# Optimization experiments

Measured on AMD Instinct MI355X. Metric: run time of the kernel, lower is better.

The kernel has to match this reference:

```python
import jax, jax.numpy as jnp
import numpy as np

N_USER = 100000
N_ITEM = 50000
N = N_USER + N_ITEM
D = 64
E = 2400000
LAYERS = 3
B = 4096


def setup_inputs() -> dict:
    key = jax.random.key(0)
    ks = jax.random.split(key, 10)
    user_emb = jax.random.normal(ks[0], (N_USER, D), dtype=jnp.float32) * 0.1
    item_emb = jax.random.normal(ks[1], (N_ITEM, D), dtype=jnp.float32) * 0.1
    graph_src = jax.random.randint(ks[2], (E,), 0, N, dtype=jnp.int32)
    graph_dst = jax.random.randint(ks[3], (E,), 0, N, dtype=jnp.int32)
    # normalized adjacency values ~ 1/deg
    graph_val = jax.random.uniform(ks[4], (E,), dtype=jnp.float32) / 16.0
    sim_src = jax.random.randint(ks[5], (E,), 0, N, dtype=jnp.int32)
    sim_dst = jax.random.randint(ks[6], (E,), 0, N, dtype=jnp.int32)
    sim_val = jax.random.uniform(ks[7], (E,), dtype=jnp.float32) / 16.0
    users = jax.random.randint(ks[8], (B,), 0, N_USER, dtype=jnp.int32)
    items = jax.random.randint(ks[9], (B,), 0, N_ITEM, dtype=jnp.int32)
    return {"user_emb": user_emb, "item_emb": item_emb,
            "graph_src": graph_src, "graph_dst": graph_dst, "graph_val": graph_val,
            "sim_src": sim_src, "sim_dst": sim_dst, "sim_val": sim_val,
            "users": users, "items": items}


def _spmm(src, dst, val, emb):
    # out[dst] += val * emb[src]  -> sparse (N,N) @ (N,D)
    return jax.ops.segment_sum(val[:, None] * emb[src], dst, num_segments=N)


def _computer(user_emb, item_emb, graph_src, graph_dst, graph_val,
              sim_src, sim_dst, sim_val):
    all_emb = jnp.concatenate([user_emb, item_emb], axis=0)  # [N, D]
    embs = [all_emb]
    for _ in range(LAYERS):
        side_emb = _spmm(graph_src, graph_dst, graph_val, all_emb)  # residual=False
        similarity_emb = _spmm(sim_src, sim_dst, sim_val, all_emb)
        att_side = jnp.exp(jnp.mean(side_emb * all_emb + side_emb, axis=1))
        att_sim = jnp.exp(jnp.mean(similarity_emb * all_emb + similarity_emb, axis=1))
        denom = att_side + att_sim
        all_emb = (att_side / denom)[:, None] * side_emb + (att_sim / denom)[:, None] * similarity_emb
        embs.append(all_emb)
    light_out = jnp.mean(jnp.stack(embs, axis=1), axis=1)  # [N, D]
    return light_out[:N_USER], light_out[N_USER:]


def reference(user_emb, item_emb, graph_src, graph_dst, graph_val,
              sim_src, sim_dst, sim_val, users, items):
    all_users, all_items = _computer(user_emb, item_emb, graph_src, graph_dst,
                                     graph_val, sim_src, sim_dst, sim_val)
    users_emb = all_users[users]  # [B, D]
    items_emb = all_items[items]  # [B, D]
    return jnp.sum(users_emb * items_emb, axis=1)  # [B]
```

## Files before the change

kernel.cpp:

```cpp
#include <hip/hip_runtime.h>
#include <hip/hip_fp16.h>

#define N_USER 100000
#define N_ITEM 50000
#define NTOT   150000
#define D      64
#define NE     2400000
#define LAYERS 3
#define BB     4096

#define NBUCK  586
#define BCAP   6144
#define PART_EDGES 6912
#define PART_GRID  ((NE + PART_EDGES - 1) / PART_EDGES)

__device__ __forceinline__ float4 h4_to_f4(uint2 u) {
    __half2 h0 = *reinterpret_cast<__half2*>(&u.x);
    __half2 h1 = *reinterpret_cast<__half2*>(&u.y);
    float2 f0 = __half22float2(h0);
    float2 f1 = __half22float2(h1);
    return make_float4(f0.x, f0.y, f1.x, f1.y);
}
__device__ __forceinline__ uint2 f4_to_h4(float4 v) {
    __half2 h0 = __float22half2_rn(make_float2(v.x, v.y));
    __half2 h1 = __float22half2_rn(make_float2(v.z, v.w));
    uint2 u;
    u.x = *reinterpret_cast<unsigned*>(&h0);
    u.y = *reinterpret_cast<unsigned*>(&h1);
    return u;
}

__global__ __launch_bounds__(256) void init_emb(const float* __restrict__ ue,
                                                const float* __restrict__ ie,
                                                float4* __restrict__ cur0,
                                                uint2*  __restrict__ cur0h) {
    int i = blockIdx.x * blockDim.x + threadIdx.x;
    const int total = NTOT * 16;
    if (i >= total) return;
    const int userElems = N_USER * 16;
    float4 v = (i < userElems) ? ((const float4*)ue)[i]
                               : ((const float4*)ie)[i - userElems];
    cur0[i]  = v;
    cur0h[i] = f4_to_h4(v);
}

__global__ __launch_bounds__(256) void partition_edges(const int*   __restrict__ gsrc,
                                                       const int*   __restrict__ gdst,
                                                       const float* __restrict__ gval,
                                                       const int*   __restrict__ ssrc,
                                                       const int*   __restrict__ sdst,
                                                       const float* __restrict__ sval,
                                                       int*  __restrict__ bucketCount,
                                                       int2* __restrict__ bucketBuf) {
    __shared__ int2 stage[PART_EDGES];
    __shared__ unsigned short bucketOf[PART_EDGES];
    __shared__ int hist[NBUCK];
    __shared__ int localBase[NBUCK];
    __shared__ int gbase[NBUCK];
    __shared__ int tsum[256];

    const int setS = (blockIdx.x >= PART_GRID) ? 1 : 0;
    const int* __restrict__ src = setS ? ssrc : gsrc;
    const int* __restrict__ dst = setS ? sdst : gdst;
    const float* __restrict__ val = setS ? sval : gval;
    const int co = setS * NBUCK;
    int bb = blockIdx.x - setS * PART_GRID;
    int lo = bb * PART_EDGES;
    int hi = min(NE, lo + PART_EDGES);
    int cnt = hi - lo;
    int tid = threadIdx.x;

    for (int i = tid; i < NBUCK; i += 256) hist[i] = 0;
    __syncthreads();
    for (int i = lo + tid; i < hi; i += 256)
        atomicAdd(&hist[dst[i] >> 8], 1);
    __syncthreads();

    int b0 = tid * 3;
    int c0 = (b0 + 0 < NBUCK) ? hist[b0 + 0] : 0;
    int c1 = (b0 + 1 < NBUCK) ? hist[b0 + 1] : 0;
    int c2 = (b0 + 2 < NBUCK) ? hist[b0 + 2] : 0;
    int mysum = c0 + c1 + c2;
    tsum[tid] = mysum;
    __syncthreads();
    #pragma unroll
    for (int off = 1; off < 256; off <<= 1) {
        int t = (tid >= off) ? tsum[tid - off] : 0;
        __syncthreads();
        tsum[tid] += t;
        __syncthreads();
    }
    int texcl = tsum[tid] - mysum;
    if (b0 + 0 < NBUCK) localBase[b0 + 0] = texcl;
    if (b0 + 1 < NBUCK) localBase[b0 + 1] = texcl + c0;
    if (b0 + 2 < NBUCK) localBase[b0 + 2] = texcl + c0 + c1;
    if (b0 + 0 < NBUCK) gbase[b0 + 0] = c0 ? atomicAdd(&bucketCount[co + b0 + 0], c0) : 0;
    if (b0 + 1 < NBUCK) gbase[b0 + 1] = c1 ? atomicAdd(&bucketCount[co + b0 + 1], c1) : 0;
    if (b0 + 2 < NBUCK) gbase[b0 + 2] = c2 ? atomicAdd(&bucketCount[co + b0 + 2], c2) : 0;
    __syncthreads();
    for (int i = tid; i < NBUCK; i += 256) hist[i] = localBase[i];
    __syncthreads();

    for (int i = lo + tid; i < hi; i += 256) {
        int d = dst[i];
        int b = d >> 8;
        int r = atomicAdd(&hist[b], 1);
        stage[r] = make_int2(src[i] | ((d & 255) << 18), __float_as_int(val[i]));
        bucketOf[r] = (unsigned short)b;
    }
    __syncthreads();

    for (int j = tid; j < cnt; j += 256) {
        int b = bucketOf[j];
        int slot = gbase[b] + (j - localBase[b]);
        if (slot < BCAP)
            bucketBuf[(size_t)(co + b) * BCAP + slot] = stage[j];
    }
}

__global__ __launch_bounds__(1024) void scan_all(const int* __restrict__ bucketCount,
                                                 int* __restrict__ bucketBase,
                                                 int* __restrict__ rpG,
                                                 int* __restrict__ rpS) {
    __shared__ int s[1024];
    int tid = threadIdx.x;
    int c = (tid < NBUCK) ? bucketCount[tid] : 0;
    s[tid] = c;
    __syncthreads();
    #pragma unroll
    for (int off = 1; off < 1024; off <<= 1) {
        int t = (tid >= off) ? s[tid - off] : 0;
        __syncthreads();
        s[tid] += t;
        __syncthreads();
    }
    if (tid < NBUCK) bucketBase[tid] = s[tid] - c;
    __syncthreads();
    int c2 = (tid < NBUCK) ? bucketCount[NBUCK + tid] : 0;
    s[tid] = c2;
    __syncthreads();
    #pragma unroll
    for (int off = 1; off < 1024; off <<= 1) {
        int t = (tid >= off) ? s[tid - off] : 0;
        __syncthreads();
        s[tid] += t;
        __syncthreads();
    }
    if (tid < NBUCK) bucketBase[NBUCK + tid] = NE + s[tid] - c2;
    if (tid == 0) { rpG[NTOT] = NE; rpS[NTOT] = 2 * NE; }
}

__global__ __launch_bounds__(256) void bucket_build(const int2* __restrict__ bucketBuf,
                                                    const int*  __restrict__ bucketCount,
                                                    const int*  __restrict__ bucketBase,
                                                    int*  __restrict__ rpG,
                                                    int*  __restrict__ rpS,
                                                    int2* __restrict__ sv) {
    __shared__ int2 e[BCAP];
    __shared__ int rhist[256];
    __shared__ int rscan[256];
    int b    = blockIdx.x;
    int setS = (b >= NBUCK) ? 1 : 0;
    int lb   = b - setS * NBUCK;
    int cnt  = min(bucketCount[b], BCAP);
    int obase = bucketBase[b];
    const int2* in = &bucketBuf[(size_t)b * BCAP];
    int tid = threadIdx.x;

    for (int i = tid; i < cnt; i += 256) e[i] = in[i];
    rhist[tid] = 0;
    __syncthreads();
    for (int i = tid; i < cnt; i += 256)
        atomicAdd(&rhist[(e[i].x >> 18) & 255], 1);
    __syncthreads();
    int myc = rhist[tid];
    rscan[tid] = myc;
    __syncthreads();
    #pragma unroll
    for (int off = 1; off < 256; off <<= 1) {
        int t = (tid >= off) ? rscan[tid - off] : 0;
        __syncthreads();
        rscan[tid] += t;
        __syncthreads();
    }
    int excl = rscan[tid] - myc;
    int grow = lb * 256 + tid;
    if (grow < NTOT) (setS ? rpS : rpG)[grow] = obase + excl;
    rhist[tid] = excl;
    __syncthreads();
    for (int i = tid; i < cnt; i += 256) {
        int row = (e[i].x >> 18) & 255;
        int pos = obase + atomicAdd(&rhist[row], 1);
        sv[pos] = make_int2(e[i].x & 0x3ffff, e[i].y);
    }
}

__global__ __launch_bounds__(256) void layer_fused(const int2* __restrict__ svG,
                                                   const int*  __restrict__ rpG,
                                                   const int2* __restrict__ svS,
                                                   const int*  __restrict__ rpS,
                                                   const float4* __restrict__ cur4,
                                                   const uint2*  __restrict__ curh,
                                                   float4* __restrict__ nxt4,
                                                   uint2*  __restrict__ nxth) {
    const int tid = threadIdx.x;
    const int lane16 = tid & 15;
    int row = blockIdx.x * 16 + (tid >> 4);
    if (row >= NTOT) return;
    size_t idx = (size_t)row * 16 + lane16;

    int pG = rpG[row], eG = rpG[row + 1];
    int pS = rpS[row], eS = rpS[row + 1];
    float4 c = cur4[idx];
    float4 aG = make_float4(0.f, 0.f, 0.f, 0.f);
    float4 aS = make_float4(0.f, 0.f, 0.f, 0.f);

    while (pG + 4 <= eG && pS + 4 <= eS) {
        int2 g0 = svG[pG + 0];
        int2 g1 = svG[pG + 1];
        int2 g2 = svG[pG + 2];
        int2 g3 = svG[pG + 3];
        int2 s0 = svS[pS + 0];
        int2 s1 = svS[pS + 1];
        int2 s2 = svS[pS + 2];
        int2 s3 = svS[pS + 3];
        uint2 ug0 = curh[(size_t)g0.x * 16 + lane16];
        uint2 ug1 = curh[(size_t)g1.x * 16 + lane16];
        uint2 ug2 = curh[(size_t)g2.x * 16 + lane16];
        uint2 ug3 = curh[(size_t)g3.x * 16 + lane16];
        uint2 us0 = curh[(size_t)s0.x * 16 + lane16];
        uint2 us1 = curh[(size_t)s1.x * 16 + lane16];
        uint2 us2 = curh[(size_t)s2.x * 16 + lane16];
        uint2 us3 = curh[(size_t)s3.x * 16 + lane16];
        float4 xg0 = h4_to_f4(ug0);
        float4 xg1 = h4_to_f4(ug1);
        float4 xg2 = h4_to_f4(ug2);
        float4 xg3 = h4_to_f4(ug3);
        float4 xs0 = h4_to_f4(us0);
        float4 xs1 = h4_to_f4(us1);
        float4 xs2 = h4_to_f4(us2);
        float4 xs3 = h4_to_f4(us3);
        float vg0 = __int_as_float(g0.y), vg1 = __int_as_float(g1.y);
        float vg2 = __int_as_float(g2.y), vg3 = __int_as_float(g3.y);
        float vs0 = __int_as_float(s0.y), vs1 = __int_as_float(s1.y);
        float vs2 = __int_as_float(s2.y), vs3 = __int_as_float(s3.y);
        aG.x = fmaf(vg0, xg0.x, aG.x); aG.y = fmaf(vg0, xg0.y, aG.y);
        aG.z = fmaf(vg0, xg0.z, aG.z); aG.w = fmaf(vg0, xg0.w, aG.w);
        aG.x = fmaf(vg1, xg1.x, aG.x); aG.y = fmaf(vg1, xg1.y, aG.y);
        aG.z = fmaf(vg1, xg1.z, aG.z); aG.w = fmaf(vg1, xg1.w, aG.w);
        aG.x = fmaf(vg2, xg2.x, aG.x); aG.y = fmaf(vg2, xg2.y, aG.y);
        aG.z = fmaf(vg2, xg2.z, aG.z); aG.w = fmaf(vg2, xg2.w, aG.w);
        aG.x = fmaf(vg3, xg3.x, aG.x); aG.y = fmaf(vg3, xg3.y, aG.y);
        aG.z = fmaf(vg3, xg3.z, aG.z); aG.w = fmaf(vg3, xg3.w, aG.w);
        aS.x = fmaf(vs0, xs0.x, aS.x); aS.y = fmaf(vs0, xs0.y, aS.y);
        aS.z = fmaf(vs0, xs0.z, aS.z); aS.w = fmaf(vs0, xs0.w, aS.w);
        aS.x = fmaf(vs1, xs1.x, aS.x); aS.y = fmaf(vs1, xs1.y, aS.y);
        aS.z = fmaf(vs1, xs1.z, aS.z); aS.w = fmaf(vs1, xs1.w, aS.w);
        aS.x = fmaf(vs2, xs2.x, aS.x); aS.y = fmaf(vs2, xs2.y, aS.y);
        aS.z = fmaf(vs2, xs2.z, aS.z); aS.w = fmaf(vs2, xs2.w, aS.w);
        aS.x = fmaf(vs3, xs3.x, aS.x); aS.y = fmaf(vs3, xs3.y, aS.y);
        aS.z = fmaf(vs3, xs3.z, aS.z); aS.w = fmaf(vs3, xs3.w, aS.w);
        pG += 4; pS += 4;
    }
    for (; pG < eG; ++pG) {
        int2 m = svG[pG];
        float4 x = h4_to_f4(curh[(size_t)m.x * 16 + lane16]);
        float v = __int_as_float(m.y);
        aG.x = fmaf(v, x.x, aG.x); aG.y = fmaf(v, x.y, aG.y);
        aG.z = fmaf(v, x.z, aG.z); aG.w = fmaf(v, x.w, aG.w);
    }
    for (; pS < eS; ++pS) {
        int2 m = svS[pS];
        float4 x = h4_to_f4(curh[(size_t)m.x * 16 + lane16]);
        float v = __int_as_float(m.y);
        aS.x = fmaf(v, x.x, aS.x); aS.y = fmaf(v, x.y, aS.y);
        aS.z = fmaf(v, x.z, aS.z); aS.w = fmaf(v, x.w, aS.w);
    }

    float4 c1 = make_float4(c.x + 1.f, c.y + 1.f, c.z + 1.f, c.w + 1.f);
    float t1 = aG.x * c1.x + aG.y * c1.y + aG.z * c1.z + aG.w * c1.w;
    float t2 = aS.x * c1.x + aS.y * c1.y + aS.z * c1.z + aS.w * c1.w;
    #pragma unroll
    for (int off = 8; off; off >>= 1) {
        t1 += __shfl_xor(t1, off, 64);
        t2 += __shfl_xor(t2, off, 64);
    }
    float a1 = expf(t1 * (1.0f / 64.0f));
    float a2 = expf(t2 * (1.0f / 64.0f));
    float den = a1 + a2;
    float w1 = a1 / den;
    float w2 = a2 / den;
    float4 nv = make_float4(w1 * aG.x + w2 * aS.x, w1 * aG.y + w2 * aS.y,
                            w1 * aG.z + w2 * aS.z, w1 * aG.w + w2 * aS.w);
    nxt4[idx] = nv;
    nxth[idx] = f4_to_h4(nv);
}

__global__ __launch_bounds__(256) void final_dot(const float* __restrict__ c0,
                                                 const float* __restrict__ c1,
                                                 const float* __restrict__ c2,
                                                 const float* __restrict__ c3,
                                                 const int* __restrict__ users,
                                                 const int* __restrict__ items,
                                                 float* __restrict__ out) {
    const int lane = threadIdx.x & 63;
    int b = blockIdx.x * (blockDim.x >> 6) + (threadIdx.x >> 6);
    if (b >= BB) return;
    size_t ub = (size_t)users[b] * D + lane;
    size_t vb = (size_t)(N_USER + items[b]) * D + lane;
    float x = (c0[ub] + c1[ub] + c2[ub] + c3[ub]) * 0.25f;
    float y = (c0[vb] + c1[vb] + c2[vb] + c3[vb]) * 0.25f;
    float p = x * y;
    #pragma unroll
    for (int off = 32; off; off >>= 1) p += __shfl_xor(p, off, 64);
    if (lane == 0) out[b] = p;
}

extern "C" void kernel_launch(void* const* d_in, const int* in_sizes, int n_in,
                              void* d_out, int out_size, void* d_ws, size_t ws_size,
                              hipStream_t stream) {
    const float* ue   = (const float*)d_in[0];
    const float* ie   = (const float*)d_in[1];
    const int*   gsrc = (const int*)d_in[2];
    const int*   gdst = (const int*)d_in[3];
    const float* gval = (const float*)d_in[4];
    const int*   ssrc = (const int*)d_in[5];
    const int*   sdst = (const int*)d_in[6];
    const float* sval = (const float*)d_in[7];
    const int*   users = (const int*)d_in[8];
    const int*   items = (const int*)d_in[9];
    float* out = (float*)d_out;

    char* p = (char*)d_ws;
    auto carve = [&](size_t bytes) { char* r = p; p += (bytes + 255) & ~(size_t)255; return r; };
    const size_t rowElems = (size_t)NTOT * D;
    float* cur[LAYERS + 1];
    for (int l = 0; l <= LAYERS; ++l) cur[l] = (float*)carve(rowElems * 4);
    uint2* curh[2];
    curh[0] = (uint2*)carve(rowElems * 2);
    curh[1] = (uint2*)carve(rowElems * 2);
    int2*  svAll = (int2*)carve((size_t)2 * NE * 8);
    int*   rpG   = (int*)carve((size_t)(NTOT + 1) * 4);
    int*   rpS   = (int*)carve((size_t)(NTOT + 1) * 4);
    int*   bucketCount = (int*)carve((size_t)2 * NBUCK * 4);
    int*   bucketBase  = (int*)carve((size_t)2 * NBUCK * 4);
    int2*  bucketBuf = (int2*)cur[2];
    (void)ws_size;

    init_emb<<<(NTOT * 16 + 255) / 256, 256, 0, stream>>>(ue, ie,
                                                          (float4*)cur[0], curh[0]);

    hipMemsetAsync(bucketCount, 0, (size_t)2 * NBUCK * 4, stream);
    partition_edges<<<2 * PART_GRID, 256, 0, stream>>>(gsrc, gdst, gval,
                                                       ssrc, sdst, sval,
                                                       bucketCount, bucketBuf);
    scan_all<<<1, 1024, 0, stream>>>(bucketCount, bucketBase, rpG, rpS);
    bucket_build<<<2 * NBUCK, 256, 0, stream>>>(bucketBuf, bucketCount, bucketBase,
                                                rpG, rpS, svAll);

    for (int l = 0; l < LAYERS; ++l) {
        layer_fused<<<(NTOT + 15) / 16, 256, 0, stream>>>(svAll, rpG, svAll, rpS,
                                                          (const float4*)cur[l],
                                                          curh[l & 1],
                                                          (float4*)cur[l + 1],
                                                          curh[(l + 1) & 1]);
    }

    final_dot<<<BB / 4, 256, 0, stream>>>(cur[0], cur[1], cur[2], cur[3],
                                          users, items, out);
}
```

Baseline: 535.0 us.

## Replace atomic bucket allocation with count/column-scan/scatter partition passes

Splits edge partitioning into a histogram pass, a per-bucket column scan over block counts, and a scatter pass that uses precomputed per-block offsets. This replaces global atomics on bucketCount with deterministic prefix offsets and drops the memset, and it unrolls the dst/src/val loads by four for more memory parallelism. The cost is two extra kernel launches, a second read of dst, and a strided column read of the block-count matrix.

New measurement: 462.7 us. 1.16x faster.

```diff
diff --git a/kernel.cpp b/kernel.cpp
--- a/kernel.cpp
+++ b/kernel.cpp
@@ -44,17 +44,109 @@
     cur0h[i] = f4_to_h4(v);
 }
 
-__global__ __launch_bounds__(256) void partition_edges(const int*   __restrict__ gsrc,
-                                                       const int*   __restrict__ gdst,
-                                                       const float* __restrict__ gval,
-                                                       const int*   __restrict__ ssrc,
-                                                       const int*   __restrict__ sdst,
-                                                       const float* __restrict__ sval,
-                                                       int*  __restrict__ bucketCount,
-                                                       int2* __restrict__ bucketBuf) {
+__global__ __launch_bounds__(256) void count_edges(const int* __restrict__ gdst,
+                                                   const int* __restrict__ sdst,
+                                                   int* __restrict__ blockCounts) {
+    __shared__ int hist[NBUCK];
+    const int setS = (blockIdx.x >= PART_GRID) ? 1 : 0;
+    const int* __restrict__ dst = setS ? sdst : gdst;
+    int bb = blockIdx.x - setS * PART_GRID;
+    int lo = bb * PART_EDGES;
+    int hi = min(NE, lo + PART_EDGES);
+    int tid = threadIdx.x;
+    for (int i = tid; i < NBUCK; i += 256) hist[i] = 0;
+    __syncthreads();
+    int i = lo + tid;
+    for (; i + 768 < hi; i += 1024) {
+        int d0 = dst[i];
+        int d1 = dst[i + 256];
+        int d2 = dst[i + 512];
+        int d3 = dst[i + 768];
+        atomicAdd(&hist[d0 >> 8], 1);
+        atomicAdd(&hist[d1 >> 8], 1);
+        atomicAdd(&hist[d2 >> 8], 1);
+        atomicAdd(&hist[d3 >> 8], 1);
+    }
+    for (; i < hi; i += 256) atomicAdd(&hist[dst[i] >> 8], 1);
+    __syncthreads();
+    int* row = &blockCounts[((size_t)blockIdx.x) * NBUCK];
+    for (int j = tid; j < NBUCK; j += 256) row[j] = hist[j];
+}
+
+__global__ __launch_bounds__(256) void colscan(const int* __restrict__ blockCounts,
+                                               int* __restrict__ blockPrefix,
+                                               int* __restrict__ bucketCount) {
+    __shared__ int s[256];
+    int tid = threadIdx.x;
+    int sb  = blockIdx.x;
+    int setS = (sb >= NBUCK) ? 1 : 0;
+    int bucket = sb - setS * NBUCK;
+    int base = 0;
+    for (int c0 = 0; c0 < PART_GRID; c0 += 256) {
+        int idx = c0 + tid;
+        size_t off = ((size_t)(setS * PART_GRID + idx)) * NBUCK + bucket;
+        int v = (idx < PART_GRID) ? blockCounts[off] : 0;
+        s[tid] = v;
+        __syncthreads();
+        #pragma unroll
+        for (int o = 1; o < 256; o <<= 1) {
+            int t = (tid >= o) ? s[tid - o] : 0;
+            __syncthreads();
+            s[tid] += t;
+            __syncthreads();
+        }
+        if (idx < PART_GRID) blockPrefix[off] = base + s[tid] - v;
+        int tot = s[255];
+        __syncthreads();
+        base += tot;
+    }
+    if (tid == 0) bucketCount[sb] = base;
+}
+
+__global__ __launch_bounds__(1024) void scan_all(const int* __restrict__ bucketCount,
+                                                 int* __restrict__ bucketBase,
+                                                 int* __restrict__ rpG,
+                                                 int* __restrict__ rpS) {
+    __shared__ int s[1024];
+    int tid = threadIdx.x;
+    int c = (tid < NBUCK) ? bucketCount[tid] : 0;
+    s[tid] = c;
+    __syncthreads();
+    #pragma unroll
+    for (int off = 1; off < 1024; off <<= 1) {
+        int t = (tid >= off) ? s[tid - off] : 0;
+        __syncthreads();
+        s[tid] += t;
+        __syncthreads();
+    }
+    if (tid < NBUCK) bucketBase[tid] = s[tid] - c;
+    __syncthreads();
+    int c2 = (tid < NBUCK) ? bucketCount[NBUCK + tid] : 0;
+    s[tid] = c2;
+    __syncthreads();
+    #pragma unroll
+    for (int off = 1; off < 1024; off <<= 1) {
+        int t = (tid >= off) ? s[tid - off] : 0;
+        __syncthreads();
+        s[tid] += t;
+        __syncthreads();
+    }
+    if (tid < NBUCK) bucketBase[NBUCK + tid] = NE + s[tid] - c2;
+    if (tid == 0) { rpG[NTOT] = NE; rpS[NTOT] = 2 * NE; }
+}
+
+__global__ __launch_bounds__(256) void partition_scatter(const int*   __restrict__ gsrc,
+                                                         const int*   __restrict__ gdst,
+                                                         const float* __restrict__ gval,
+                                                         const int*   __restrict__ ssrc,
+                                                         const int*   __restrict__ sdst,
+                                                         const float* __restrict__ sval,
+                                                         const int*   __restrict__ blockCounts,
+                                                         const int*   __restrict__ blockPrefix,
+                                                         int2* __restrict__ bucketBuf) {
     __shared__ int2 stage[PART_EDGES];
     __shared__ unsigned short bucketOf[PART_EDGES];
-    __shared__ int hist[NBUCK];
+    __shared__ int cursor[NBUCK];
     __shared__ int localBase[NBUCK];
     __shared__ int gbase[NBUCK];
     __shared__ int tsum[256];
@@ -69,17 +161,12 @@
     int hi = min(NE, lo + PART_EDGES);
     int cnt = hi - lo;
     int tid = threadIdx.x;
-
-    for (int i = tid; i < NBUCK; i += 256) hist[i] = 0;
-    __syncthreads();
-    for (int i = lo + tid; i < hi; i += 256)
-        atomicAdd(&hist[dst[i] >> 8], 1);
-    __syncthreads();
+    size_t rowOff = (size_t)blockIdx.x * NBUCK;
 
     int b0 = tid * 3;
-    int c0 = (b0 + 0 < NBUCK) ? hist[b0 + 0] : 0;
-    int c1 = (b0 + 1 < NBUCK) ? hist[b0 + 1] : 0;
-    int c2 = (b0 + 2 < NBUCK) ? hist[b0 + 2] : 0;
+    int c0 = (b0 + 0 < NBUCK) ? blockCounts[rowOff + b0 + 0] : 0;
+    int c1 = (b0 + 1 < NBUCK) ? blockCounts[rowOff + b0 + 1] : 0;
+    int c2 = (b0 + 2 < NBUCK) ? blockCounts[rowOff + b0 + 2] : 0;
     int mysum = c0 + c1 + c2;
     tsum[tid] = mysum;
     __syncthreads();
@@ -91,20 +178,55 @@
         __syncthreads();
     }
     int texcl = tsum[tid] - mysum;
-    if (b0 + 0 < NBUCK) localBase[b0 + 0] = texcl;
-    if (b0 + 1 < NBUCK) localBase[b0 + 1] = texcl + c0;
-    if (b0 + 2 < NBUCK) localBase[b0 + 2] = texcl + c0 + c1;
-    if (b0 + 0 < NBUCK) gbase[b0 + 0] = c0 ? atomicAdd(&bucketCount[co + b0 + 0], c0) : 0;
-    if (b0 + 1 < NBUCK) gbase[b0 + 1] = c1 ? atomicAdd(&bucketCount[co + b0 + 1], c1) : 0;
-    if (b0 + 2 < NBUCK) gbase[b0 + 2] = c2 ? atomicAdd(&bucketCount[co + b0 + 2], c2) : 0;
-    __syncthreads();
-    for (int i = tid; i < NBUCK; i += 256) hist[i] = localBase[i];
-    __syncthreads();
-
-    for (int i = lo + tid; i < hi; i += 256) {
+    if (b0 + 0 < NBUCK) {
+        localBase[b0 + 0] = texcl;
+        cursor[b0 + 0]    = texcl;
+        gbase[b0 + 0]     = blockPrefix[rowOff + b0 + 0];
+    }
+    if (b0 + 1 < NBUCK) {
+        localBase[b0 + 1] = texcl + c0;
+        cursor[b0 + 1]    = texcl + c0;
+        gbase[b0 + 1]     = blockPrefix[rowOff + b0 + 1];
+    }
+    if (b0 + 2 < NBUCK) {
+        localBase[b0 + 2] = texcl + c0 + c1;
+        cursor[b0 + 2]    = texcl + c0 + c1;
+        gbase[b0 + 2]     = blockPrefix[rowOff + b0 + 2];
+    }
+    __syncthreads();
+
+    int i = lo + tid;
+    for (; i + 768 < hi; i += 1024) {
+        int d0 = dst[i];
+        int d1 = dst[i + 256];
+        int d2 = dst[i + 512];
+        int d3 = dst[i + 768];
+        int s0 = src[i];
+        int s1 = src[i + 256];
+        int s2 = src[i + 512];
+        int s3 = src[i + 768];
+        float v0 = val[i];
+        float v1 = val[i + 256];
+        float v2 = val[i + 512];
+        float v3 = val[i + 768];
+        int k0 = d0 >> 8, k1 = d1 >> 8, k2 = d2 >> 8, k3 = d3 >> 8;
+        int r0 = atomicAdd(&cursor[k0], 1);
+        int r1 = atomicAdd(&cursor[k1], 1);
+        int r2 = atomicAdd(&cursor[k2], 1);
+        int r3 = atomicAdd(&cursor[k3], 1);
+        stage[r0] = make_int2(s0 | ((d0 & 255) << 18), __float_as_int(v0));
+        stage[r1] = make_int2(s1 | ((d1 & 255) << 18), __float_as_int(v1));
+        stage[r2] = make_int2(s2 | ((d2 & 255) << 18), __float_as_int(v2));
+        stage[r3] = make_int2(s3 | ((d3 & 255) << 18), __float_as_int(v3));
+        bucketOf[r0] = (unsigned short)k0;
+        bucketOf[r1] = (unsigned short)k1;
+        bucketOf[r2] = (unsigned short)k2;
+        bucketOf[r3] = (unsigned short)k3;
+    }
+    for (; i < hi; i += 256) {
         int d = dst[i];
         int b = d >> 8;
-        int r = atomicAdd(&hist[b], 1);
+        int r = atomicAdd(&cursor[b], 1);
         stage[r] = make_int2(src[i] | ((d & 255) << 18), __float_as_int(val[i]));
         bucketOf[r] = (unsigned short)b;
     }
@@ -116,38 +238,6 @@
         if (slot < BCAP)
             bucketBuf[(size_t)(co + b) * BCAP + slot] = stage[j];
     }
-}
-
-__global__ __launch_bounds__(1024) void scan_all(const int* __restrict__ bucketCount,
-                                                 int* __restrict__ bucketBase,
-                                                 int* __restrict__ rpG,
-                                                 int* __restrict__ rpS) {
-    __shared__ int s[1024];
-    int tid = threadIdx.x;
-    int c = (tid < NBUCK) ? bucketCount[tid] : 0;
-    s[tid] = c;
-    __syncthreads();
-    #pragma unroll
-    for (int off = 1; off < 1024; off <<= 1) {
-        int t = (tid >= off) ? s[tid - off] : 0;
-        __syncthreads();
-        s[tid] += t;
-        __syncthreads();
-    }
-    if (tid < NBUCK) bucketBase[tid] = s[tid] - c;
-    __syncthreads();
-    int c2 = (tid < NBUCK) ? bucketCount[NBUCK + tid] : 0;
-    s[tid] = c2;
-    __syncthreads();
-    #pragma unroll
-    for (int off = 1; off < 1024; off <<= 1) {
-        int t = (tid >= off) ? s[tid - off] : 0;
-        __syncthreads();
-        s[tid] += t;
-        __syncthreads();
-    }
-    if (tid < NBUCK) bucketBase[NBUCK + tid] = NE + s[tid] - c2;
-    if (tid == 0) { rpG[NTOT] = NE; rpS[NTOT] = 2 * NE; }
 }
 
 __global__ __launch_bounds__(256) void bucket_build(const int2* __restrict__ bucketBuf,
@@ -344,17 +434,21 @@
     int*   rpS   = (int*)carve((size_t)(NTOT + 1) * 4);
     int*   bucketCount = (int*)carve((size_t)2 * NBUCK * 4);
     int*   bucketBase  = (int*)carve((size_t)2 * NBUCK * 4);
+    int*   blockCounts = (int*)carve((size_t)2 * PART_GRID * NBUCK * 4);
+    int*   blockPrefix = (int*)carve((size_t)2 * PART_GRID * NBUCK * 4);
     int2*  bucketBuf = (int2*)cur[2];
     (void)ws_size;
 
     init_emb<<<(NTOT * 16 + 255) / 256, 256, 0, stream>>>(ue, ie,
                                                           (float4*)cur[0], curh[0]);
 
-    hipMemsetAsync(bucketCount, 0, (size_t)2 * NBUCK * 4, stream);
-    partition_edges<<<2 * PART_GRID, 256, 0, stream>>>(gsrc, gdst, gval,
-                                                       ssrc, sdst, sval,
-                                                       bucketCount, bucketBuf);
+    count_edges<<<2 * PART_GRID, 256, 0, stream>>>(gdst, sdst, blockCounts);
+    colscan<<<2 * NBUCK, 256, 0, stream>>>(blockCounts, blockPrefix, bucketCount);
     scan_all<<<1, 1024, 0, stream>>>(bucketCount, bucketBase, rpG, rpS);
+    partition_scatter<<<2 * PART_GRID, 256, 0, stream>>>(gsrc, gdst, gval,
+                                                         ssrc, sdst, sval,
+                                                         blockCounts, blockPrefix,
+                                                         bucketBuf);
     bucket_build<<<2 * NBUCK, 256, 0, stream>>>(bucketBuf, bucketCount, bucketBase,
                                                 rpG, rpS, svAll);
 
```
